# Optimization experiments

Hardware: AMD Instinct MI355X
Metric: run time of the kernel (lower is better)

Reference implementation:

```python
import jax, jax.numpy as jnp
import numpy as np

COORD_DIM = 4
HIDDEN = 256
N_HIDDEN_LAYERS = 4  # num_layers - 1 hidden->hidden layers after the first
MIN_OMEGA = 10.0
MAX_OMEGA = 100.0
MEDIAN_OMEGA = (MIN_OMEGA + MAX_OMEGA) / 2.0
N = 524288


def _uniform(key, shape, bound):
    return jax.random.uniform(key, shape, jnp.float32, -bound, bound)


def setup_inputs() -> dict:
    key = jax.random.key(0)
    ks = jax.random.split(key, 16)
    coords = jax.random.normal(ks[0], (N, COORD_DIM), jnp.float32)
    # omega predictor: Linear(4, 64) -> ReLU -> Linear(64, 1) -> Sigmoid
    ow1 = _uniform(ks[1], (COORD_DIM, HIDDEN // 4), 1.0 / np.sqrt(COORD_DIM))
    ob1 = _uniform(ks[2], (HIDDEN // 4,), 1.0 / np.sqrt(COORD_DIM))
    ow2 = _uniform(ks[3], (HIDDEN // 4, 1), 1.0 / np.sqrt(HIDDEN // 4))
    ob2 = _uniform(ks[4], (1,), 1.0 / np.sqrt(HIDDEN // 4))
    # SIREN first layer: uniform(-1/in_features, 1/in_features)
    w0 = _uniform(ks[5], (COORD_DIM, HIDDEN), 1.0 / COORD_DIM)
    b0 = _uniform(ks[6], (HIDDEN,), 1.0 / np.sqrt(COORD_DIM))
    # SIREN hidden layers: uniform(-sqrt(6/in)/omega0, ...), stacked [4, 256, 256]
    hb = np.sqrt(6.0 / HIDDEN) / MEDIAN_OMEGA
    wh = _uniform(ks[7], (N_HIDDEN_LAYERS, HIDDEN, HIDDEN), hb)
    bh = _uniform(ks[8], (N_HIDDEN_LAYERS, HIDDEN), 1.0 / np.sqrt(HIDDEN))
    wf = _uniform(ks[9], (HIDDEN, 1), hb)
    bf = _uniform(ks[10], (1,), 1.0 / np.sqrt(HIDDEN))
    return {"coords": coords, "ow1": ow1, "ob1": ob1, "ow2": ow2, "ob2": ob2,
            "w0": w0, "b0": b0, "wh": wh, "bh": bh, "wf": wf, "bf": bf}


def reference(coords, ow1, ob1, ow2, ob2, w0, b0, wh, bh, wf, bf):
    # adaptive omega per coordinate: [N, 1]
    h = jax.nn.relu(coords @ ow1 + ob1)
    omega = MIN_OMEGA + (MAX_OMEGA - MIN_OMEGA) * jax.nn.sigmoid(h @ ow2 + ob2)
    # SIREN stack: x = sin(omega * (x @ W + b))
    x = jnp.sin(omega * (coords @ w0 + b0))
    for i in range(N_HIDDEN_LAYERS):
        x = jnp.sin(omega * (x @ wh[i] + bh[i]))
    return x @ wf + bf  # [N, 1]
```

## Files before the change

### kernel.cpp

```cpp
#include <hip/hip_runtime.h>
#include <hip/hip_bf16.h>

typedef _Float16 f16;
typedef f16 f16x4 __attribute__((ext_vector_type(4)));
typedef f16 f16x8 __attribute__((ext_vector_type(8)));
typedef __fp16 h16x2 __attribute__((ext_vector_type(2)));
typedef __fp16 h16x4 __attribute__((ext_vector_type(4)));
typedef float f32x4 __attribute__((ext_vector_type(4)));
typedef float f32x16 __attribute__((ext_vector_type(16)));

#define MT 128
#define LDST 260
#define INV2PI 0.15915494309189535f

__global__ __launch_bounds__(64)
void prep_wt(const float* __restrict__ wh, f16* __restrict__ wt) {
    const int b = blockIdx.x;
    const int layer = b >> 7, wcblk = (b >> 4) & 7, kblk = b & 15;
    const int lane = threadIdx.x;
    const int l31 = lane & 31, lh = lane >> 5;
    const float* src = wh + layer * 65536 + (kblk * 16 + lh * 8) * 256 + wcblk * 32 + l31;
    f16x8 v;
#pragma unroll
    for (int j = 0; j < 8; j++) v[j] = (f16)src[j * 256];
    *(f16x8*)(wt + b * 512 + lane * 8) = v;
}

__device__ inline f16x8 lds_ld8(const f16* p) {
    f16x4 lo = *(const f16x4*)p;
    f16x4 hi = *(const f16x4*)(p + 4);
    return __builtin_shufflevector(lo, hi, 0, 1, 2, 3, 4, 5, 6, 7);
}

__device__ inline f16x4 pk4(float z0, float z1, float z2, float z3) {
    h16x2 a = __builtin_amdgcn_cvt_pkrtz(z0, z1);
    h16x2 b = __builtin_amdgcn_cvt_pkrtz(z2, z3);
    h16x4 r = __builtin_shufflevector(a, b, 0, 1, 2, 3);
    return __builtin_bit_cast(f16x4, r);
}

__global__ __launch_bounds__(512, 4)
void siren_fused(const float* __restrict__ coords,
                 const float* __restrict__ ow1, const float* __restrict__ ob1,
                 const float* __restrict__ ow2, const float* __restrict__ ob2,
                 const float* __restrict__ w0, const float* __restrict__ b0,
                 const f16* __restrict__ wt,
                 const float* __restrict__ bh,
                 const float* __restrict__ wf,
                 const float* __restrict__ bf,
                 float* __restrict__ out) {
    __shared__ __align__(16) f16 Xs[MT * LDST];
    __shared__ float om_rev[MT];
    __shared__ __align__(16) float crd[MT * 4];
    __shared__ __align__(16) float wf_s[256];

    const int t = threadIdx.x;
    const long base_pt = (long)blockIdx.x * MT;

    if (t < MT) ((f32x4*)crd)[t] = ((const f32x4*)(coords + base_pt * 4))[t];
    if (t < 256) wf_s[t] = wf[t];
    __syncthreads();

    if (t < MT) {
        const float c0 = crd[t * 4], c1 = crd[t * 4 + 1], c2 = crd[t * 4 + 2], c3 = crd[t * 4 + 3];
        float h[64];
#pragma unroll
        for (int j = 0; j < 64; j++) {
            float z = ob1[j] + c0 * ow1[j] + c1 * ow1[64 + j] + c2 * ow1[128 + j] + c3 * ow1[192 + j];
            h[j] = fmaxf(z, 0.f);
        }
        float z2 = ob2[0];
#pragma unroll
        for (int j = 0; j < 64; j++) z2 += h[j] * ow2[j];
        const float sig = 1.f / (1.f + __expf(-z2));
        om_rev[t] = (10.f + 90.f * sig) * INV2PI;
    }
    __syncthreads();

    {
        const int pt = t >> 2;
        const int q = t & 3;
        const float c0 = crd[pt * 4], c1 = crd[pt * 4 + 1], c2 = crd[pt * 4 + 2], c3 = crd[pt * 4 + 3];
        const float orv = om_rev[pt];
#pragma unroll
        for (int i = 0; i < 4; i++) {
            const int ch = (q + 4 * i) * 16;
#pragma unroll
            for (int c = 0; c < 16; c += 4) {
                f32x4 wv0 = *(const f32x4*)(w0 + 0 * 256 + ch + c);
                f32x4 wv1 = *(const f32x4*)(w0 + 1 * 256 + ch + c);
                f32x4 wv2 = *(const f32x4*)(w0 + 2 * 256 + ch + c);
                f32x4 wv3 = *(const f32x4*)(w0 + 3 * 256 + ch + c);
                f32x4 bv  = *(const f32x4*)(b0 + ch + c);
                float z[4];
#pragma unroll
                for (int j = 0; j < 4; j++) {
                    float zz = bv[j] + c0 * wv0[j] + c1 * wv1[j] + c2 * wv2[j] + c3 * wv3[j];
                    z[j] = __builtin_amdgcn_sinf(orv * zz);
                }
                *(f16x4*)&Xs[pt * LDST + ch + c] = pk4(z[0], z[1], z[2], z[3]);
            }
        }
    }
    __syncthreads();

    const int lane = t & 63;
    const int wave = t >> 6;
    const int l31 = lane & 31;
    const int lh = lane >> 5;
    const int wc0 = wave * 32;

#pragma unroll 1
    for (int layer = 0; layer < 4; layer++) {
        const f16* afrag = wt + ((layer * 8 + wave) * 16) * 512 + lane * 8;
        const f16* bptr = &Xs[l31 * LDST + lh * 8];

        f32x16 acc[4];
#pragma unroll
        for (int g = 0; g < 4; g++) {
            f32x4 bb = *(const f32x4*)(bh + layer * 256 + wc0 + g * 8 + lh * 4);
#pragma unroll
            for (int r = 0; r < 4; r++)
#pragma unroll
                for (int j = 0; j < 4; j++) acc[r][g * 4 + j] = bb[j];
        }

        f16x8 a[2];
        a[0] = *(const f16x8*)(afrag);
        a[1] = *(const f16x8*)(afrag + 512);

#pragma unroll 4
        for (int kb = 0; kb < 16; kb++) {
            const int s = kb & 1;
            f16x8 av = a[s];
            if (kb + 2 < 16)
                a[s] = *(const f16x8*)(afrag + (kb + 2) * 512);
            f16x8 bv0 = lds_ld8(bptr + 0 * 32 * LDST + kb * 16);
            f16x8 bv1 = lds_ld8(bptr + 1 * 32 * LDST + kb * 16);
            f16x8 bv2 = lds_ld8(bptr + 2 * 32 * LDST + kb * 16);
            f16x8 bv3 = lds_ld8(bptr + 3 * 32 * LDST + kb * 16);
            acc[0] = __builtin_amdgcn_mfma_f32_32x32x16_f16(av, bv0, acc[0], 0, 0, 0);
            acc[1] = __builtin_amdgcn_mfma_f32_32x32x16_f16(av, bv1, acc[1], 0, 0, 0);
            acc[2] = __builtin_amdgcn_mfma_f32_32x32x16_f16(av, bv2, acc[2], 0, 0, 0);
            acc[3] = __builtin_amdgcn_mfma_f32_32x32x16_f16(av, bv3, acc[3], 0, 0, 0);
        }
        __syncthreads();

        float orv[4];
#pragma unroll
        for (int r = 0; r < 4; r++) orv[r] = om_rev[r * 32 + l31];
#pragma unroll
        for (int g = 0; g < 4; g++) {
            const int wc = wc0 + g * 8 + lh * 4;
#pragma unroll
            for (int r = 0; r < 4; r++) {
                const int prow = r * 32 + l31;
                float z[4];
#pragma unroll
                for (int j = 0; j < 4; j++)
                    z[j] = __builtin_amdgcn_sinf(orv[r] * acc[r][g * 4 + j]);
                *(f16x4*)&Xs[prow * LDST + wc] = pk4(z[0], z[1], z[2], z[3]);
            }
        }
        __syncthreads();
    }

    {
        const int pt = t >> 2;
        const int q = t & 3;
        const f16* xrow = &Xs[pt * LDST];
        float s = 0.f;
#pragma unroll
        for (int i = 0; i < 4; i++) {
            const int ch = (q + 4 * i) * 16;
#pragma unroll
            for (int c = 0; c < 16; c += 4) {
                f16x4 xv = *(const f16x4*)(xrow + ch + c);
                f32x4 wv = *(const f32x4*)&wf_s[ch + c];
                s += (float)xv[0] * wv[0] + (float)xv[1] * wv[1]
                   + (float)xv[2] * wv[2] + (float)xv[3] * wv[3];
            }
        }
        s += __shfl_xor(s, 1, 64);
        s += __shfl_xor(s, 2, 64);
        if (q == 0) out[base_pt + pt] = s + bf[0];
    }
}

extern "C" void kernel_launch(void* const* d_in, const int* in_sizes, int n_in,
                              void* d_out, int out_size, void* d_ws, size_t ws_size,
                              hipStream_t stream) {
    (void)in_sizes; (void)n_in; (void)out_size; (void)ws_size;
    const float* coords = (const float*)d_in[0];
    const float* ow1 = (const float*)d_in[1];
    const float* ob1 = (const float*)d_in[2];
    const float* ow2 = (const float*)d_in[3];
    const float* ob2 = (const float*)d_in[4];
    const float* w0  = (const float*)d_in[5];
    const float* b0  = (const float*)d_in[6];
    const float* wh  = (const float*)d_in[7];
    const float* bh  = (const float*)d_in[8];
    const float* wf  = (const float*)d_in[9];
    const float* bf  = (const float*)d_in[10];
    float* out = (float*)d_out;
    f16* wt = (f16*)d_ws;

    prep_wt<<<512, 64, 0, stream>>>(wh, wt);
    siren_fused<<<524288 / MT, 512, 0, stream>>>(coords, ow1, ob1, ow2, ob2,
                                                 w0, b0, wt, bh, wf, bf, out);
}
```

Measured before the change: 446.0 us.

## Restructure SIREN kernel around 16x16x32 MFMA, register-resident weights, double-buffered LDS

Cuts the point tile from 128 to 64 per block and switches from 32x32x16 to 16x16x32 MFMAs. Each wave now holds its whole weight slice for a layer in registers and prefetches the next layer's weights while the sine epilogue runs. The activation buffer in LDS is double-buffered, which removes one barrier per layer. The omega MLP is spread across all threads with shuffle reductions instead of 128 threads doing serial loops. In exchange the kernel uses more registers, which may lower occupancy, and smaller tiles reuse each weight load less.

```diff
diff --git a/kernel.cpp b/kernel.cpp
--- a/kernel.cpp
+++ b/kernel.cpp
@@ -7,29 +7,22 @@
 typedef __fp16 h16x2 __attribute__((ext_vector_type(2)));
 typedef __fp16 h16x4 __attribute__((ext_vector_type(4)));
 typedef float f32x4 __attribute__((ext_vector_type(4)));
-typedef float f32x16 __attribute__((ext_vector_type(16)));
-
-#define MT 128
-#define LDST 260
+
+#define MT 64
+#define LDST 264
 #define INV2PI 0.15915494309189535f
 
 __global__ __launch_bounds__(64)
 void prep_wt(const float* __restrict__ wh, f16* __restrict__ wt) {
     const int b = blockIdx.x;
-    const int layer = b >> 7, wcblk = (b >> 4) & 7, kblk = b & 15;
-    const int lane = threadIdx.x;
-    const int l31 = lane & 31, lh = lane >> 5;
-    const float* src = wh + layer * 65536 + (kblk * 16 + lh * 8) * 256 + wcblk * 32 + l31;
+    const int layer = b >> 7, cblk = (b >> 3) & 15, kb = b & 7;
+    const int L = threadIdx.x;
+    const int l15 = L & 15, g4 = L >> 4;
+    const float* src = wh + layer * 65536 + (kb * 32 + g4 * 8) * 256 + cblk * 16 + l15;
     f16x8 v;
 #pragma unroll
     for (int j = 0; j < 8; j++) v[j] = (f16)src[j * 256];
-    *(f16x8*)(wt + b * 512 + lane * 8) = v;
-}
-
-__device__ inline f16x8 lds_ld8(const f16* p) {
-    f16x4 lo = *(const f16x4*)p;
-    f16x4 hi = *(const f16x4*)(p + 4);
-    return __builtin_shufflevector(lo, hi, 0, 1, 2, 3, 4, 5, 6, 7);
+    *(f16x8*)(wt + b * 512 + L * 8) = v;
 }
 
 __device__ inline f16x4 pk4(float z0, float z1, float z2, float z3) {
@@ -49,7 +42,7 @@
                  const float* __restrict__ wf,
                  const float* __restrict__ bf,
                  float* __restrict__ out) {
-    __shared__ __align__(16) f16 Xs[MT * LDST];
+    __shared__ __align__(16) f16 Xs[2][MT * LDST];
     __shared__ float om_rev[MT];
     __shared__ __align__(16) float crd[MT * 4];
     __shared__ __align__(16) float wf_s[256];
@@ -61,128 +54,138 @@
     if (t < 256) wf_s[t] = wf[t];
     __syncthreads();
 
-    if (t < MT) {
-        const float c0 = crd[t * 4], c1 = crd[t * 4 + 1], c2 = crd[t * 4 + 2], c3 = crd[t * 4 + 3];
-        float h[64];
-#pragma unroll
-        for (int j = 0; j < 64; j++) {
+    {
+        const int pt = t >> 3, q = t & 7;
+        const float c0 = crd[pt * 4], c1 = crd[pt * 4 + 1], c2 = crd[pt * 4 + 2], c3 = crd[pt * 4 + 3];
+        float z2p = 0.f;
+#pragma unroll
+        for (int jj = 0; jj < 8; jj++) {
+            const int j = q * 8 + jj;
             float z = ob1[j] + c0 * ow1[j] + c1 * ow1[64 + j] + c2 * ow1[128 + j] + c3 * ow1[192 + j];
-            h[j] = fmaxf(z, 0.f);
-        }
-        float z2 = ob2[0];
-#pragma unroll
-        for (int j = 0; j < 64; j++) z2 += h[j] * ow2[j];
-        const float sig = 1.f / (1.f + __expf(-z2));
-        om_rev[t] = (10.f + 90.f * sig) * INV2PI;
+            z2p += fmaxf(z, 0.f) * ow2[j];
+        }
+        z2p += __shfl_xor(z2p, 1, 64);
+        z2p += __shfl_xor(z2p, 2, 64);
+        z2p += __shfl_xor(z2p, 4, 64);
+        if (q == 0) {
+            const float sig = 1.f / (1.f + __expf(-(z2p + ob2[0])));
+            om_rev[pt] = (10.f + 90.f * sig) * INV2PI;
+        }
+    }
+
+    const int lane = t & 63;
+    const int wave = t >> 6;
+    const int l15 = lane & 15;
+    const int g4 = lane >> 4;
+    const int wc0 = wave * 32;
+
+    f16x8 a0[8], a1[8];
+    {
+        const f16* af = wt + (wave * 2 * 8) * 512 + lane * 8;
+#pragma unroll
+        for (int kb = 0; kb < 8; kb++) {
+            a0[kb] = *(const f16x8*)(af + kb * 512);
+            a1[kb] = *(const f16x8*)(af + 4096 + kb * 512);
+        }
     }
     __syncthreads();
 
     {
-        const int pt = t >> 2;
-        const int q = t & 3;
+        const int pt = t >> 3, q = t & 7;
         const float c0 = crd[pt * 4], c1 = crd[pt * 4 + 1], c2 = crd[pt * 4 + 2], c3 = crd[pt * 4 + 3];
         const float orv = om_rev[pt];
 #pragma unroll
-        for (int i = 0; i < 4; i++) {
-            const int ch = (q + 4 * i) * 16;
-#pragma unroll
-            for (int c = 0; c < 16; c += 4) {
-                f32x4 wv0 = *(const f32x4*)(w0 + 0 * 256 + ch + c);
-                f32x4 wv1 = *(const f32x4*)(w0 + 1 * 256 + ch + c);
-                f32x4 wv2 = *(const f32x4*)(w0 + 2 * 256 + ch + c);
-                f32x4 wv3 = *(const f32x4*)(w0 + 3 * 256 + ch + c);
-                f32x4 bv  = *(const f32x4*)(b0 + ch + c);
-                float z[4];
-#pragma unroll
-                for (int j = 0; j < 4; j++) {
-                    float zz = bv[j] + c0 * wv0[j] + c1 * wv1[j] + c2 * wv2[j] + c3 * wv3[j];
-                    z[j] = __builtin_amdgcn_sinf(orv * zz);
-                }
-                *(f16x4*)&Xs[pt * LDST + ch + c] = pk4(z[0], z[1], z[2], z[3]);
+        for (int c = 0; c < 32; c += 4) {
+            const int ch = q * 32 + c;
+            f32x4 wv0 = *(const f32x4*)(w0 + 0 * 256 + ch);
+            f32x4 wv1 = *(const f32x4*)(w0 + 1 * 256 + ch);
+            f32x4 wv2 = *(const f32x4*)(w0 + 2 * 256 + ch);
+            f32x4 wv3 = *(const f32x4*)(w0 + 3 * 256 + ch);
+            f32x4 bv  = *(const f32x4*)(b0 + ch);
+            float z[4];
+#pragma unroll
+            for (int j = 0; j < 4; j++) {
+                float zz = bv[j] + c0 * wv0[j] + c1 * wv1[j] + c2 * wv2[j] + c3 * wv3[j];
+                z[j] = __builtin_amdgcn_sinf(orv * zz);
             }
+            *(f16x4*)&Xs[0][pt * LDST + ch] = pk4(z[0], z[1], z[2], z[3]);
         }
     }
     __syncthreads();
-
-    const int lane = t & 63;
-    const int wave = t >> 6;
-    const int l31 = lane & 31;
-    const int lh = lane >> 5;
-    const int wc0 = wave * 32;
 
 #pragma unroll 1
     for (int layer = 0; layer < 4; layer++) {
-        const f16* afrag = wt + ((layer * 8 + wave) * 16) * 512 + lane * 8;
-        const f16* bptr = &Xs[l31 * LDST + lh * 8];
-
-        f32x16 acc[4];
-#pragma unroll
-        for (int g = 0; g < 4; g++) {
-            f32x4 bb = *(const f32x4*)(bh + layer * 256 + wc0 + g * 8 + lh * 4);
-#pragma unroll
-            for (int r = 0; r < 4; r++)
-#pragma unroll
-                for (int j = 0; j < 4; j++) acc[r][g * 4 + j] = bb[j];
-        }
-
-        f16x8 a[2];
-        a[0] = *(const f16x8*)(afrag);
-        a[1] = *(const f16x8*)(afrag + 512);
-
-#pragma unroll 4
-        for (int kb = 0; kb < 16; kb++) {
-            const int s = kb & 1;
-            f16x8 av = a[s];
-            if (kb + 2 < 16)
-                a[s] = *(const f16x8*)(afrag + (kb + 2) * 512);
-            f16x8 bv0 = lds_ld8(bptr + 0 * 32 * LDST + kb * 16);
-            f16x8 bv1 = lds_ld8(bptr + 1 * 32 * LDST + kb * 16);
-            f16x8 bv2 = lds_ld8(bptr + 2 * 32 * LDST + kb * 16);
-            f16x8 bv3 = lds_ld8(bptr + 3 * 32 * LDST + kb * 16);
-            acc[0] = __builtin_amdgcn_mfma_f32_32x32x16_f16(av, bv0, acc[0], 0, 0, 0);
-            acc[1] = __builtin_amdgcn_mfma_f32_32x32x16_f16(av, bv1, acc[1], 0, 0, 0);
-            acc[2] = __builtin_amdgcn_mfma_f32_32x32x16_f16(av, bv2, acc[2], 0, 0, 0);
-            acc[3] = __builtin_amdgcn_mfma_f32_32x32x16_f16(av, bv3, acc[3], 0, 0, 0);
+        const int cur = layer & 1;
+
+        f32x4 acc[4][2];
+#pragma unroll
+        for (int ct = 0; ct < 2; ct++) {
+            const f32x4 bb = *(const f32x4*)(bh + layer * 256 + wc0 + ct * 16 + g4 * 4);
+#pragma unroll
+            for (int rt = 0; rt < 4; rt++) acc[rt][ct] = bb;
+        }
+
+        const f16* bp = &Xs[cur][l15 * LDST + g4 * 8];
+
+        __builtin_amdgcn_s_setprio(1);
+#pragma unroll
+        for (int kb = 0; kb < 8; kb++) {
+            f16x8 bv0 = *(const f16x8*)(bp + 0 * 16 * LDST + kb * 32);
+            f16x8 bv1 = *(const f16x8*)(bp + 1 * 16 * LDST + kb * 32);
+            acc[0][0] = __builtin_amdgcn_mfma_f32_16x16x32_f16(a0[kb], bv0, acc[0][0], 0, 0, 0);
+            acc[0][1] = __builtin_amdgcn_mfma_f32_16x16x32_f16(a1[kb], bv0, acc[0][1], 0, 0, 0);
+            acc[1][0] = __builtin_amdgcn_mfma_f32_16x16x32_f16(a0[kb], bv1, acc[1][0], 0, 0, 0);
+            acc[1][1] = __builtin_amdgcn_mfma_f32_16x16x32_f16(a1[kb], bv1, acc[1][1], 0, 0, 0);
+            f16x8 bv2 = *(const f16x8*)(bp + 2 * 16 * LDST + kb * 32);
+            f16x8 bv3 = *(const f16x8*)(bp + 3 * 16 * LDST + kb * 32);
+            acc[2][0] = __builtin_amdgcn_mfma_f32_16x16x32_f16(a0[kb], bv2, acc[2][0], 0, 0, 0);
+            acc[2][1] = __builtin_amdgcn_mfma_f32_16x16x32_f16(a1[kb], bv2, acc[2][1], 0, 0, 0);
+            acc[3][0] = __builtin_amdgcn_mfma_f32_16x16x32_f16(a0[kb], bv3, acc[3][0], 0, 0, 0);
+            acc[3][1] = __builtin_amdgcn_mfma_f32_16x16x32_f16(a1[kb], bv3, acc[3][1], 0, 0, 0);
+        }
+        __builtin_amdgcn_s_setprio(0);
+
+        if (layer < 3) {
+            const f16* af = wt + (((layer + 1) * 16 + wave * 2) * 8) * 512 + lane * 8;
+#pragma unroll
+            for (int kb = 0; kb < 8; kb++) {
+                a0[kb] = *(const f16x8*)(af + kb * 512);
+                a1[kb] = *(const f16x8*)(af + 4096 + kb * 512);
+            }
+        }
+
+        float orv[4];
+#pragma unroll
+        for (int rt = 0; rt < 4; rt++) orv[rt] = om_rev[rt * 16 + l15];
+#pragma unroll
+        for (int ct = 0; ct < 2; ct++) {
+            const int ch = wc0 + ct * 16 + g4 * 4;
+#pragma unroll
+            for (int rt = 0; rt < 4; rt++) {
+                float z[4];
+#pragma unroll
+                for (int j = 0; j < 4; j++)
+                    z[j] = __builtin_amdgcn_sinf(orv[rt] * acc[rt][ct][j]);
+                *(f16x4*)&Xs[cur ^ 1][(rt * 16 + l15) * LDST + ch] = pk4(z[0], z[1], z[2], z[3]);
+            }
         }
         __syncthreads();
-
-        float orv[4];
-#pragma unroll
-        for (int r = 0; r < 4; r++) orv[r] = om_rev[r * 32 + l31];
-#pragma unroll
-        for (int g = 0; g < 4; g++) {
-            const int wc = wc0 + g * 8 + lh * 4;
-#pragma unroll
-            for (int r = 0; r < 4; r++) {
-                const int prow = r * 32 + l31;
-                float z[4];
-#pragma unroll
-                for (int j = 0; j < 4; j++)
-                    z[j] = __builtin_amdgcn_sinf(orv[r] * acc[r][g * 4 + j]);
-                *(f16x4*)&Xs[prow * LDST + wc] = pk4(z[0], z[1], z[2], z[3]);
-            }
-        }
-        __syncthreads();
-    }
-
-    {
-        const int pt = t >> 2;
-        const int q = t & 3;
-        const f16* xrow = &Xs[pt * LDST];
+    }
+
+    {
+        const int pt = t >> 3, q = t & 7;
+        const f16* xrow = &Xs[0][pt * LDST + q * 32];
         float s = 0.f;
 #pragma unroll
-        for (int i = 0; i < 4; i++) {
-            const int ch = (q + 4 * i) * 16;
-#pragma unroll
-            for (int c = 0; c < 16; c += 4) {
-                f16x4 xv = *(const f16x4*)(xrow + ch + c);
-                f32x4 wv = *(const f32x4*)&wf_s[ch + c];
-                s += (float)xv[0] * wv[0] + (float)xv[1] * wv[1]
-                   + (float)xv[2] * wv[2] + (float)xv[3] * wv[3];
-            }
+        for (int c = 0; c < 32; c += 4) {
+            f16x4 xv = *(const f16x4*)(xrow + c);
+            f32x4 wv = *(const f32x4*)&wf_s[q * 32 + c];
+            s += (float)xv[0] * wv[0] + (float)xv[1] * wv[1]
+               + (float)xv[2] * wv[2] + (float)xv[3] * wv[3];
         }
         s += __shfl_xor(s, 1, 64);
         s += __shfl_xor(s, 2, 64);
+        s += __shfl_xor(s, 4, 64);
         if (q == 0) out[base_pt + pt] = s + bf[0];
     }
 }
```

After: 553.0 us. +24.0%, slower.

## Halve point tile, hold whole layer weights in registers, parallelize omega MLP

Applied to the files above, without the earlier changes.

The point tile drops from 128 to 64 points per block. Each wave now preloads all 16 weight fragments of a layer into registers and prefetches the next layer's fragments during the epilogue, instead of using a two-deep rolling global load. The omega predictor is split across 8 threads per point with shuffle reductions rather than one thread per point. The intent is to shorten the serial prologue, get more blocks in flight and hide weight-load latency. The cost is twice as many weight reloads per point, fewer MFMAs per A fragment, and higher register pressure.

```diff
diff --git a/kernel.cpp b/kernel.cpp
--- a/kernel.cpp
+++ b/kernel.cpp
@@ -9,7 +9,7 @@
 typedef float f32x4 __attribute__((ext_vector_type(4)));
 typedef float f32x16 __attribute__((ext_vector_type(16)));
 
-#define MT 128
+#define MT 64
 #define LDST 260
 #define INV2PI 0.15915494309189535f
 
@@ -57,132 +57,134 @@
     const int t = threadIdx.x;
     const long base_pt = (long)blockIdx.x * MT;
 
-    if (t < MT) ((f32x4*)crd)[t] = ((const f32x4*)(coords + base_pt * 4))[t];
-    if (t < 256) wf_s[t] = wf[t];
-    __syncthreads();
-
-    if (t < MT) {
-        const float c0 = crd[t * 4], c1 = crd[t * 4 + 1], c2 = crd[t * 4 + 2], c3 = crd[t * 4 + 3];
-        float h[64];
-#pragma unroll
-        for (int j = 0; j < 64; j++) {
-            float z = ob1[j] + c0 * ow1[j] + c1 * ow1[64 + j] + c2 * ow1[128 + j] + c3 * ow1[192 + j];
-            h[j] = fmaxf(z, 0.f);
-        }
-        float z2 = ob2[0];
-#pragma unroll
-        for (int j = 0; j < 64; j++) z2 += h[j] * ow2[j];
-        const float sig = 1.f / (1.f + __expf(-z2));
-        om_rev[t] = (10.f + 90.f * sig) * INV2PI;
-    }
-    __syncthreads();
-
-    {
-        const int pt = t >> 2;
-        const int q = t & 3;
-        const float c0 = crd[pt * 4], c1 = crd[pt * 4 + 1], c2 = crd[pt * 4 + 2], c3 = crd[pt * 4 + 3];
-        const float orv = om_rev[pt];
-#pragma unroll
-        for (int i = 0; i < 4; i++) {
-            const int ch = (q + 4 * i) * 16;
-#pragma unroll
-            for (int c = 0; c < 16; c += 4) {
-                f32x4 wv0 = *(const f32x4*)(w0 + 0 * 256 + ch + c);
-                f32x4 wv1 = *(const f32x4*)(w0 + 1 * 256 + ch + c);
-                f32x4 wv2 = *(const f32x4*)(w0 + 2 * 256 + ch + c);
-                f32x4 wv3 = *(const f32x4*)(w0 + 3 * 256 + ch + c);
-                f32x4 bv  = *(const f32x4*)(b0 + ch + c);
-                float z[4];
-#pragma unroll
-                for (int j = 0; j < 4; j++) {
-                    float zz = bv[j] + c0 * wv0[j] + c1 * wv1[j] + c2 * wv2[j] + c3 * wv3[j];
-                    z[j] = __builtin_amdgcn_sinf(orv * zz);
-                }
-                *(f16x4*)&Xs[pt * LDST + ch + c] = pk4(z[0], z[1], z[2], z[3]);
-            }
-        }
-    }
-    __syncthreads();
-
     const int lane = t & 63;
     const int wave = t >> 6;
     const int l31 = lane & 31;
     const int lh = lane >> 5;
     const int wc0 = wave * 32;
 
+    if (t < MT) ((f32x4*)crd)[t] = ((const f32x4*)(coords + base_pt * 4))[t];
+    if (t < 256) wf_s[t] = wf[t];
+    __syncthreads();
+
+    {
+        const int pt = t >> 3, q = t & 7;
+        const float c0 = crd[pt * 4], c1 = crd[pt * 4 + 1], c2 = crd[pt * 4 + 2], c3 = crd[pt * 4 + 3];
+        float z2p = 0.f;
+#pragma unroll
+        for (int jj = 0; jj < 8; jj++) {
+            const int j = q * 8 + jj;
+            float z = ob1[j] + c0 * ow1[j] + c1 * ow1[64 + j] + c2 * ow1[128 + j] + c3 * ow1[192 + j];
+            z2p += fmaxf(z, 0.f) * ow2[j];
+        }
+        z2p += __shfl_xor(z2p, 1, 64);
+        z2p += __shfl_xor(z2p, 2, 64);
+        z2p += __shfl_xor(z2p, 4, 64);
+        if (q == 0) {
+            const float sig = 1.f / (1.f + __expf(-(z2p + ob2[0])));
+            om_rev[pt] = (10.f + 90.f * sig) * INV2PI;
+        }
+    }
+
+    f16x8 a[16];
+    {
+        const f16* af = wt + ((0 * 8 + wave) * 16) * 512 + lane * 8;
+#pragma unroll
+        for (int kb = 0; kb < 16; kb++) a[kb] = *(const f16x8*)(af + kb * 512);
+    }
+    __syncthreads();
+
+    {
+        const int pt = t >> 3, q = t & 7;
+        const float c0 = crd[pt * 4], c1 = crd[pt * 4 + 1], c2 = crd[pt * 4 + 2], c3 = crd[pt * 4 + 3];
+        const float orv = om_rev[pt];
+#pragma unroll
+        for (int i = 0; i < 2; i++) {
+            const int ch0 = (q + 8 * i) * 16;
+#pragma unroll
+            for (int c = 0; c < 16; c += 4) {
+                const int ch = ch0 + c;
+                f32x4 wv0 = *(const f32x4*)(w0 + 0 * 256 + ch);
+                f32x4 wv1 = *(const f32x4*)(w0 + 1 * 256 + ch);
+                f32x4 wv2 = *(const f32x4*)(w0 + 2 * 256 + ch);
+                f32x4 wv3 = *(const f32x4*)(w0 + 3 * 256 + ch);
+                f32x4 bv  = *(const f32x4*)(b0 + ch);
+                float z[4];
+#pragma unroll
+                for (int j = 0; j < 4; j++) {
+                    float zz = bv[j] + c0 * wv0[j] + c1 * wv1[j] + c2 * wv2[j] + c3 * wv3[j];
+                    z[j] = __builtin_amdgcn_sinf(orv * zz);
+                }
+                *(f16x4*)&Xs[pt * LDST + ch] = pk4(z[0], z[1], z[2], z[3]);
+            }
+        }
+    }
+    __syncthreads();
+
 #pragma unroll 1
     for (int layer = 0; layer < 4; layer++) {
-        const f16* afrag = wt + ((layer * 8 + wave) * 16) * 512 + lane * 8;
-        const f16* bptr = &Xs[l31 * LDST + lh * 8];
-
-        f32x16 acc[4];
+        f32x16 acc[2];
 #pragma unroll
         for (int g = 0; g < 4; g++) {
             f32x4 bb = *(const f32x4*)(bh + layer * 256 + wc0 + g * 8 + lh * 4);
 #pragma unroll
-            for (int r = 0; r < 4; r++)
-#pragma unroll
-                for (int j = 0; j < 4; j++) acc[r][g * 4 + j] = bb[j];
-        }
-
-        f16x8 a[2];
-        a[0] = *(const f16x8*)(afrag);
-        a[1] = *(const f16x8*)(afrag + 512);
-
-#pragma unroll 4
+            for (int j = 0; j < 4; j++) {
+                acc[0][g * 4 + j] = bb[j];
+                acc[1][g * 4 + j] = bb[j];
+            }
+        }
+
+        const f16* bptr = &Xs[l31 * LDST + lh * 8];
+
+#pragma unroll
         for (int kb = 0; kb < 16; kb++) {
-            const int s = kb & 1;
-            f16x8 av = a[s];
-            if (kb + 2 < 16)
-                a[s] = *(const f16x8*)(afrag + (kb + 2) * 512);
             f16x8 bv0 = lds_ld8(bptr + 0 * 32 * LDST + kb * 16);
             f16x8 bv1 = lds_ld8(bptr + 1 * 32 * LDST + kb * 16);
-            f16x8 bv2 = lds_ld8(bptr + 2 * 32 * LDST + kb * 16);
-            f16x8 bv3 = lds_ld8(bptr + 3 * 32 * LDST + kb * 16);
-            acc[0] = __builtin_amdgcn_mfma_f32_32x32x16_f16(av, bv0, acc[0], 0, 0, 0);
-            acc[1] = __builtin_amdgcn_mfma_f32_32x32x16_f16(av, bv1, acc[1], 0, 0, 0);
-            acc[2] = __builtin_amdgcn_mfma_f32_32x32x16_f16(av, bv2, acc[2], 0, 0, 0);
-            acc[3] = __builtin_amdgcn_mfma_f32_32x32x16_f16(av, bv3, acc[3], 0, 0, 0);
+            acc[0] = __builtin_amdgcn_mfma_f32_32x32x16_f16(a[kb], bv0, acc[0], 0, 0, 0);
+            acc[1] = __builtin_amdgcn_mfma_f32_32x32x16_f16(a[kb], bv1, acc[1], 0, 0, 0);
+        }
+
+        if (layer < 3) {
+            const f16* af = wt + (((layer + 1) * 8 + wave) * 16) * 512 + lane * 8;
+#pragma unroll
+            for (int kb = 0; kb < 16; kb++) a[kb] = *(const f16x8*)(af + kb * 512);
         }
         __syncthreads();
 
-        float orv[4];
-#pragma unroll
-        for (int r = 0; r < 4; r++) orv[r] = om_rev[r * 32 + l31];
+        const float orv0 = om_rev[l31];
+        const float orv1 = om_rev[32 + l31];
 #pragma unroll
         for (int g = 0; g < 4; g++) {
             const int wc = wc0 + g * 8 + lh * 4;
-#pragma unroll
-            for (int r = 0; r < 4; r++) {
-                const int prow = r * 32 + l31;
-                float z[4];
-#pragma unroll
-                for (int j = 0; j < 4; j++)
-                    z[j] = __builtin_amdgcn_sinf(orv[r] * acc[r][g * 4 + j]);
-                *(f16x4*)&Xs[prow * LDST + wc] = pk4(z[0], z[1], z[2], z[3]);
-            }
+            float z[4];
+#pragma unroll
+            for (int j = 0; j < 4; j++) z[j] = __builtin_amdgcn_sinf(orv0 * acc[0][g * 4 + j]);
+            *(f16x4*)&Xs[(0 * 32 + l31) * LDST + wc] = pk4(z[0], z[1], z[2], z[3]);
+#pragma unroll
+            for (int j = 0; j < 4; j++) z[j] = __builtin_amdgcn_sinf(orv1 * acc[1][g * 4 + j]);
+            *(f16x4*)&Xs[(1 * 32 + l31) * LDST + wc] = pk4(z[0], z[1], z[2], z[3]);
         }
         __syncthreads();
     }
 
     {
-        const int pt = t >> 2;
-        const int q = t & 3;
+        const int pt = t >> 3, q = t & 7;
         const f16* xrow = &Xs[pt * LDST];
         float s = 0.f;
 #pragma unroll
-        for (int i = 0; i < 4; i++) {
-            const int ch = (q + 4 * i) * 16;
+        for (int i = 0; i < 2; i++) {
+            const int ch0 = (q + 8 * i) * 16;
 #pragma unroll
             for (int c = 0; c < 16; c += 4) {
-                f16x4 xv = *(const f16x4*)(xrow + ch + c);
-                f32x4 wv = *(const f32x4*)&wf_s[ch + c];
+                f16x4 xv = *(const f16x4*)(xrow + ch0 + c);
+                f32x4 wv = *(const f32x4*)&wf_s[ch0 + c];
                 s += (float)xv[0] * wv[0] + (float)xv[1] * wv[1]
                    + (float)xv[2] * wv[2] + (float)xv[3] * wv[3];
             }
         }
         s += __shfl_xor(s, 1, 64);
         s += __shfl_xor(s, 2, 64);
+        s += __shfl_xor(s, 4, 64);
         if (q == 0) out[base_pt + pt] = s + bf[0];
     }
 }
```

Measured after the change: 473.3 us. 6.1% more time.
